# Kernel tuning notes

Measured on AMD Instinct MI355X. Metric: run time of the kernel, lower is better.

## Reference

```python
import jax, jax.numpy as jnp
import numpy as np

B, T, C = 2, 2048, 1024
H = 16
HD = C // H  # 64


def setup_inputs() -> dict:
    key = jax.random.key(0)
    ks = jax.random.split(key, 6)
    s_in = 1.0 / np.sqrt(C)
    s_pr = 1.0 / np.sqrt(H * HD)
    x = jax.random.normal(ks[0], (B, T, C), dtype=jnp.float32)
    Wq = jax.random.uniform(ks[1], (H, C, HD), jnp.float32, -s_in, s_in)
    Wk = jax.random.uniform(ks[2], (H, C, HD), jnp.float32, -s_in, s_in)
    Wv = jax.random.uniform(ks[3], (H, C, HD), jnp.float32, -s_in, s_in)
    Wp = jax.random.uniform(ks[4], (H * HD, C), jnp.float32, -s_pr, s_pr)
    bp = jax.random.uniform(ks[5], (C,), jnp.float32, -s_pr, s_pr)
    return {"x": x, "Wq": Wq, "Wk": Wk, "Wv": Wv, "Wp": Wp, "bp": bp}


def reference(x, Wq, Wk, Wv, Wp, bp):
    # per-head projections: [B,T,C] x [H,C,D] -> [B,H,T,D]
    q = jnp.einsum('btc,hcd->bhtd', x, Wq)
    k = jnp.einsum('btc,hcd->bhtd', x, Wk)
    v = jnp.einsum('btc,hcd->bhtd', x, Wv)
    scale = HD ** (-0.5)
    scores = jnp.einsum('bhtd,bhsd->bhts', q, k) * scale  # [B,H,T,T]
    causal = jnp.tril(jnp.ones((T, T), dtype=bool))
    scores = jnp.where(causal, scores, -jnp.inf)
    w = jax.nn.softmax(scores, axis=-1)
    out = jnp.einsum('bhts,bhsd->bhtd', w, v)  # [B,H,T,D]
    # concat heads: [B,T,H*D] (head order matches torch.cat over heads)
    out = jnp.transpose(out, (0, 2, 1, 3)).reshape(B, T, H * HD)
    return out @ Wp + bp
```

## Files before the change

### kernel.cpp

```cpp
#include <hip/hip_runtime.h>
#include <hip/hip_bf16.h>

#define B_NUM 2
#define T_SEQ 2048
#define C_DIM 1024
#define H_NUM 16
#define HD    64
#define M_TOT 4096
#define BH_N  32

typedef __attribute__((ext_vector_type(8))) short short8;
typedef __attribute__((ext_vector_type(4))) float floatx4;

__device__ __forceinline__ short f2bf(float f) {
    unsigned u = __float_as_uint(f);
    u += 0x7FFFu + ((u >> 16) & 1u);
    return (short)(u >> 16);
}

__device__ __forceinline__ unsigned pk2bf(float a, float b) {
    float2 f2; f2.x = a; f2.y = b;
    __hip_bfloat162 h = __float22bfloat162_rn(f2);
    unsigned u; __builtin_memcpy(&u, &h, 4); return u;
}

__device__ __forceinline__ void gld16(const short* g, short* l) {
    __builtin_amdgcn_global_load_lds(
        (const __attribute__((address_space(1))) void*)g,
        (__attribute__((address_space(3))) void*)l, 16, 0, 0);
}

__global__ __launch_bounds__(256) void prep_k(
    const float* __restrict__ x, const float* __restrict__ Wq,
    const float* __restrict__ Wk, const float* __restrict__ Wv,
    const float* __restrict__ Wp,
    short* __restrict__ xb, short* __restrict__ wt, short* __restrict__ wpt) {
    const int bid = blockIdx.x;
    const int tid = threadIdx.x;
    if (bid < 2048) {
        int idx = (bid * 256 + tid) * 8;
        float4 a = *(const float4*)(x + idx);
        float4 b = *(const float4*)(x + idx + 4);
        short8 o;
        o[0] = f2bf(a.x); o[1] = f2bf(a.y); o[2] = f2bf(a.z); o[3] = f2bf(a.w);
        o[4] = f2bf(b.x); o[5] = f2bf(b.y); o[6] = f2bf(b.z); o[7] = f2bf(b.w);
        *(short8*)(xb + idx) = o;
        return;
    }
    const int b2 = bid - 2048;
    const int ct = b2 & 15, y = b2 >> 4;
    __shared__ float shf[4096];

    const float* src;
    size_t src_stride;
    int src_col0;
    short* dst;
    int dst_col0;
    if (y < 48) {
        const int which = y >> 4, h = y & 15;
        src = ((which == 0) ? Wq : (which == 1) ? Wk : Wv)
              + (size_t)h * C_DIM * HD + (size_t)(ct * 64) * HD;
        src_stride = HD;  src_col0 = 0;
        dst = wt + (size_t)((which * 16 + h) * 64) * C_DIM;
        dst_col0 = ct * 64;
    } else {
        const int nt = y - 48;
        src = Wp + (size_t)(ct * 64) * C_DIM;
        src_stride = C_DIM;  src_col0 = nt * 64;
        dst = wpt + (size_t)(nt * 64) * C_DIM;
        dst_col0 = ct * 64;
    }
    #pragma unroll
    for (int p = 0; p < 4; ++p) {
        int idx = tid + 256 * p;
        int c = idx >> 4, d4 = idx & 15;
        float4 v = *(const float4*)(src + (size_t)c * src_stride + src_col0 + d4 * 4);
        shf[(d4 * 4 + 0) * 64 + (c ^ (d4 * 4 + 0))] = v.x;
        shf[(d4 * 4 + 1) * 64 + (c ^ (d4 * 4 + 1))] = v.y;
        shf[(d4 * 4 + 2) * 64 + (c ^ (d4 * 4 + 2))] = v.z;
        shf[(d4 * 4 + 3) * 64 + (c ^ (d4 * 4 + 3))] = v.w;
    }
    __syncthreads();
    #pragma unroll
    for (int p = 0; p < 2; ++p) {
        int idx = tid + 256 * p;
        int d = idx >> 3, cc = idx & 7;
        const float* row = shf + d * 64;
        uint4 u;
        u.x = pk2bf(row[(cc * 8 + 0) ^ d], row[(cc * 8 + 1) ^ d]);
        u.y = pk2bf(row[(cc * 8 + 2) ^ d], row[(cc * 8 + 3) ^ d]);
        u.z = pk2bf(row[(cc * 8 + 4) ^ d], row[(cc * 8 + 5) ^ d]);
        u.w = pk2bf(row[(cc * 8 + 6) ^ d], row[(cc * 8 + 7) ^ d]);
        *(uint4*)(dst + (size_t)d * C_DIM + dst_col0 + cc * 8) = u;
    }
}

__global__ __launch_bounds__(512, 2) void qkv_k(
    const short* __restrict__ xb, const short* __restrict__ wt,
    short* __restrict__ qb, short* __restrict__ kb, short* __restrict__ vtb) {
    const int swz = (blockIdx.x & 7) * 24 + (blockIdx.x >> 3);
    const int mt = swz / 12, ntg = swz % 12;
    const int m0 = mt * 256, n0 = ntg * 256;
    const int which = n0 >> 10;
    const float sc = (which == 0) ? 0.125f * 1.4426950408889634f : 1.0f;

    __shared__ short smem[32768];
    short* As = smem;
    short* Bs = smem + 16384;

    const int tid = threadIdx.x;
    const int lane = tid & 63, w = tid >> 6;
    const int wm = w & 1, wn = w >> 1;
    const int hi = lane >> 4, llo = lane & 15;
    const int lrow = lane >> 3;
    const int lswz = ((lane & 7) ^ (lrow & 7)) * 8;
    const int fc0 = (hi ^ (llo & 7)) * 8;
    const int fc1 = ((hi + 4) ^ (llo & 7)) * 8;

    floatx4 acc[8][4];
    #pragma unroll
    for (int i = 0; i < 8; ++i)
        #pragma unroll
        for (int j = 0; j < 4; ++j)
            #pragma unroll
            for (int r = 0; r < 4; ++r) acc[i][j][r] = 0.0f;

    const size_t a_base = (size_t)(m0 + w * 32 + lrow) * C_DIM + lswz;
    const size_t b_base = (size_t)(n0 + w * 32 + lrow) * C_DIM + lswz;

    for (int kt = 0; kt < C_DIM / 64; ++kt) {
        const int c0 = kt * 64;
        __syncthreads();
        #pragma unroll
        for (int p = 0; p < 4; ++p) {
            gld16(xb + a_base + (size_t)p * 8 * C_DIM + c0, &As[(w * 32 + p * 8) * 64]);
            gld16(wt + b_base + (size_t)p * 8 * C_DIM + c0, &Bs[(w * 32 + p * 8) * 64]);
        }
        __syncthreads();

        short8 bf[4][2];
        #pragma unroll
        for (int ni = 0; ni < 4; ++ni) {
            const int row = wn * 64 + ni * 16 + llo;
            bf[ni][0] = *(const short8*)(&Bs[row * 64 + fc0]);
            bf[ni][1] = *(const short8*)(&Bs[row * 64 + fc1]);
        }
        #pragma unroll
        for (int mi = 0; mi < 8; ++mi) {
            const int row = wm * 128 + mi * 16 + llo;
            short8 a0 = *(const short8*)(&As[row * 64 + fc0]);
            short8 a1 = *(const short8*)(&As[row * 64 + fc1]);
            #pragma unroll
            for (int ni = 0; ni < 4; ++ni) {
                acc[mi][ni] = __builtin_amdgcn_mfma_f32_16x16x32_bf16(a0, bf[ni][0], acc[mi][ni], 0, 0, 0);
                acc[mi][ni] = __builtin_amdgcn_mfma_f32_16x16x32_bf16(a1, bf[ni][1], acc[mi][ni], 0, 0, 0);
            }
        }
    }

    const int bb = m0 >> 11;
    if (which < 2) {
        short (*R)[76] = (short(*)[76])smem;
        short* outp = (which == 0) ? qb : kb;
        #pragma unroll
        for (int c = 0; c < 4; ++c) {
            __syncthreads();
            if (wn == c) {
                #pragma unroll
                for (int mi = 0; mi < 8; ++mi)
                    #pragma unroll
                    for (int ni = 0; ni < 4; ++ni)
                        #pragma unroll
                        for (int r = 0; r < 4; ++r)
                            R[wm * 128 + mi * 16 + hi * 4 + r][ni * 16 + llo] =
                                f2bf(acc[mi][ni][r] * sc);
            }
            __syncthreads();
            const int h = ((n0 + c * 64) >> 6) & 15;
            #pragma unroll
            for (int p = 0; p < 4; ++p) {
                int idx = tid + 512 * p;
                int r = idx >> 3, cc = idx & 7;
                short8 vv = *(const short8*)(&R[r][cc * 8]);
                int t = (m0 + r) & 2047;
                *(short8*)(outp + ((size_t)(bb * H_NUM + h) * T_SEQ + t) * HD + cc * 8) = vv;
            }
        }
    } else {
        short (*R2)[268] = (short(*)[268])smem;
        #pragma unroll
        for (int c = 0; c < 4; ++c) {
            __syncthreads();
            if (wn == c) {
                #pragma unroll
                for (int mi = 0; mi < 8; ++mi)
                    #pragma unroll
                    for (int ni = 0; ni < 4; ++ni)
                        #pragma unroll
                        for (int r = 0; r < 4; ++r)
                            R2[ni * 16 + llo][wm * 128 + mi * 16 + hi * 4 + r] =
                                f2bf(acc[mi][ni][r]);
            }
            __syncthreads();
            const int h = ((n0 + c * 64) >> 6) & 15;
            #pragma unroll
            for (int p = 0; p < 4; ++p) {
                int idx = tid + 512 * p;
                int d = idx >> 5, cc = idx & 31;
                short8 vv = *(const short8*)(&R2[d][cc * 8]);
                *(short8*)(vtb + ((size_t)((bb * H_NUM + h) * HD + d)) * T_SEQ
                           + (m0 & 2047) + cc * 8) = vv;
            }
        }
    }
}

__global__ __launch_bounds__(512) void attn_k(
    const short* __restrict__ qb, const short* __restrict__ kb,
    const short* __restrict__ vtb, short* __restrict__ attb) {
    const int bh = blockIdx.x;
    const int y = blockIdx.y;
    const int qt = (y < 8) ? (15 - y) : (y - 8);
    const int b = bh >> 4, h = bh & 15;
    const short* K  = kb  + (size_t)bh * T_SEQ * HD;
    const short* Vt = vtb + (size_t)bh * HD * T_SEQ;

    __shared__ short Ks[2][4096];
    __shared__ short Vs[2][4096];
    __shared__ short Ps[128][76];

    const int tid = threadIdx.x;
    const int lane = tid & 63, w = tid >> 6;
    const int hi = lane >> 4, llo = lane & 15;
    const int lrow = lane >> 3;
    const int lswz = ((lane & 7) ^ (lrow & 7)) * 8;
    const int fc0 = (hi ^ (llo & 7)) * 8;
    const int fc1 = ((hi + 4) ^ (llo & 7)) * 8;
    const int kmax = 2 * qt + 1;

    short8 qf[2];
    const int qcol0 = qt * 128 + w * 16;
    #pragma unroll
    for (int kh = 0; kh < 2; ++kh)
        qf[kh] = *(const short8*)(qb +
            ((size_t)bh * T_SEQ + qcol0 + llo) * HD + kh * 32 + hi * 8);

    short8 av4;
    #pragma unroll
    for (int j = 0; j < 8; ++j) av4[j] = (llo == 0) ? (short)0x3F80 : (short)0;

    gld16(K + (size_t)(w * 8 + lrow) * HD + lswz, &Ks[0][(w * 8) * 64]);
    gld16(Vt + (size_t)(w * 8 + lrow) * T_SEQ + lswz, &Vs[0][(w * 8) * 64]);

    floatx4 Oa[5];
    #pragma unroll
    for (int n = 0; n < 5; ++n)
        #pragma unroll
        for (int r = 0; r < 4; ++r) Oa[n][r] = 0.0f;

    for (int kt = 0; kt <= kmax; ++kt) {
        __syncthreads();
        const int buf = kt & 1;

        if (kt + 1 <= kmax) {
            const int s0 = (kt + 1) * 64;
            const int nb = buf ^ 1;
            gld16(K + ((size_t)s0 + w * 8 + lrow) * HD + lswz, &Ks[nb][(w * 8) * 64]);
            gld16(Vt + (size_t)(w * 8 + lrow) * T_SEQ + s0 + lswz, &Vs[nb][(w * 8) * 64]);
        }

        short8 ak[4][2];
        #pragma unroll
        for (int nt = 0; nt < 4; ++nt) {
            const int row = nt * 16 + llo;
            ak[nt][0] = *(const short8*)(&Ks[buf][row * 64 + fc0]);
            ak[nt][1] = *(const short8*)(&Ks[buf][row * 64 + fc1]);
        }
        floatx4 sf[4];
        #pragma unroll
        for (int nt = 0; nt < 4; ++nt)
            #pragma unroll
            for (int r = 0; r < 4; ++r) sf[nt][r] = 0.0f;
        __builtin_amdgcn_s_setprio(1);
        #pragma unroll
        for (int nt = 0; nt < 4; ++nt)
            #pragma unroll
            for (int kh = 0; kh < 2; ++kh)
                sf[nt] = __builtin_amdgcn_mfma_f32_16x16x32_bf16(
                    ak[nt][kh], qf[kh], sf[nt], 0, 0, 0);
        __builtin_amdgcn_s_setprio(0);

        const int sbase = kt * 64;
        if (sbase + 63 > qcol0) {
            const int qlane = qcol0 + llo;
            #pragma unroll
            for (int nt = 0; nt < 4; ++nt)
                #pragma unroll
                for (int r = 0; r < 4; ++r)
                    if (sbase + nt * 16 + hi * 4 + r > qlane) sf[nt][r] = -3.0e38f;
        }

        #pragma unroll
        for (int nt = 0; nt < 4; ++nt) {
            float p0 = __builtin_amdgcn_exp2f(sf[nt][0]);
            float p1 = __builtin_amdgcn_exp2f(sf[nt][1]);
            float p2 = __builtin_amdgcn_exp2f(sf[nt][2]);
            float p3 = __builtin_amdgcn_exp2f(sf[nt][3]);
            uint2 u; u.x = pk2bf(p0, p1); u.y = pk2bf(p2, p3);
            *(uint2*)(&Ps[w * 16 + llo][nt * 16 + hi * 4]) = u;
        }

        short8 av[5][2];
        #pragma unroll
        for (int nt2 = 0; nt2 < 4; ++nt2) {
            const int row = nt2 * 16 + llo;
            av[nt2][0] = *(const short8*)(&Vs[buf][row * 64 + fc0]);
            av[nt2][1] = *(const short8*)(&Vs[buf][row * 64 + fc1]);
        }
        av[4][0] = av4;
        av[4][1] = av4;
        short8 bpf[2];
        #pragma unroll
        for (int kh = 0; kh < 2; ++kh)
            bpf[kh] = *(const short8*)(&Ps[w * 16 + llo][kh * 32 + hi * 8]);
        __builtin_amdgcn_s_setprio(1);
        #pragma unroll
        for (int nt2 = 0; nt2 < 5; ++nt2)
            #pragma unroll
            for (int kh = 0; kh < 2; ++kh)
                Oa[nt2] = __builtin_amdgcn_mfma_f32_16x16x32_bf16(
                    av[nt2][kh], bpf[kh], Oa[nt2], 0, 0, 0);
        __builtin_amdgcn_s_setprio(0);
    }

    {
        float lb = __shfl(Oa[4][0], llo);
        float inv = 1.0f / lb;
        #pragma unroll
        for (int nt2 = 0; nt2 < 4; ++nt2) {
            uint2 u;
            u.x = pk2bf(Oa[nt2][0] * inv, Oa[nt2][1] * inv);
            u.y = pk2bf(Oa[nt2][2] * inv, Oa[nt2][3] * inv);
            *(uint2*)(&Ps[w * 16 + llo][nt2 * 16 + hi * 4]) = u;
        }
    }
    __syncthreads();
    #pragma unroll
    for (int p = 0; p < 2; ++p) {
        int idx = tid + 512 * p;
        int r = idx >> 3, cc = idx & 7;
        short8 vv = *(const short8*)(&Ps[r][cc * 8]);
        *(short8*)(attb + ((size_t)(b * T_SEQ + qt * 128 + r)) * C_DIM + h * HD + cc * 8) = vv;
    }
}

__global__ __launch_bounds__(256) void proj_k(
    const short* __restrict__ attb, const short* __restrict__ wpt,
    const float* __restrict__ bp, float* __restrict__ out) {
    const int mt = blockIdx.x, ntg = blockIdx.y;
    const int m0 = mt * 128, n0 = ntg * 128;

    __shared__ short smem[16384];
    short* As = smem;
    short* Bs = smem + 8192;

    const int tid = threadIdx.x;
    const int lane = tid & 63, w = tid >> 6;
    const int wm = w & 1, wn = w >> 1;
    const int hi = lane >> 4, llo = lane & 15;
    const int lrow = lane >> 3;
    const int lswz = ((lane & 7) ^ (lrow & 7)) * 8;
    const int fc0 = (hi ^ (llo & 7)) * 8;
    const int fc1 = ((hi + 4) ^ (llo & 7)) * 8;

    floatx4 acc[4][4];
    #pragma unroll
    for (int i = 0; i < 4; ++i)
        #pragma unroll
        for (int j = 0; j < 4; ++j)
            #pragma unroll
            for (int r = 0; r < 4; ++r) acc[i][j][r] = 0.0f;

    const size_t a_base = (size_t)(m0 + w * 32 + lrow) * C_DIM + lswz;
    const size_t b_base = (size_t)(n0 + w * 32 + lrow) * C_DIM + lswz;

    for (int kt = 0; kt < C_DIM / 64; ++kt) {
        const int c0 = kt * 64;
        __syncthreads();
        #pragma unroll
        for (int p = 0; p < 4; ++p) {
            gld16(attb + a_base + (size_t)p * 8 * C_DIM + c0, &As[(w * 32 + p * 8) * 64]);
            gld16(wpt  + b_base + (size_t)p * 8 * C_DIM + c0, &Bs[(w * 32 + p * 8) * 64]);
        }
        __syncthreads();

        short8 af[4][2];
        #pragma unroll
        for (int mi = 0; mi < 4; ++mi) {
            const int row = wm * 64 + mi * 16 + llo;
            af[mi][0] = *(const short8*)(&As[row * 64 + fc0]);
            af[mi][1] = *(const short8*)(&As[row * 64 + fc1]);
        }
        #pragma unroll
        for (int ni = 0; ni < 4; ++ni) {
            const int row = wn * 64 + ni * 16 + llo;
            short8 b0 = *(const short8*)(&Bs[row * 64 + fc0]);
            short8 b1 = *(const short8*)(&Bs[row * 64 + fc1]);
            #pragma unroll
            for (int mi = 0; mi < 4; ++mi) {
                acc[mi][ni] = __builtin_amdgcn_mfma_f32_16x16x32_bf16(af[mi][0], b0, acc[mi][ni], 0, 0, 0);
                acc[mi][ni] = __builtin_amdgcn_mfma_f32_16x16x32_bf16(af[mi][1], b1, acc[mi][ni], 0, 0, 0);
            }
        }
    }

    #pragma unroll
    for (int ni = 0; ni < 4; ++ni) {
        const int n = n0 + wn * 64 + ni * 16 + llo;
        const float bias = bp[n];
        #pragma unroll
        for (int mi = 0; mi < 4; ++mi)
            #pragma unroll
            for (int r = 0; r < 4; ++r) {
                int m = m0 + wm * 64 + mi * 16 + hi * 4 + r;
                out[(size_t)m * C_DIM + n] = acc[mi][ni][r] + bias;
            }
    }
}

extern "C" void kernel_launch(void* const* d_in, const int* in_sizes, int n_in,
                              void* d_out, int out_size, void* d_ws, size_t ws_size,
                              hipStream_t stream) {
    const float* x  = (const float*)d_in[0];
    const float* Wq = (const float*)d_in[1];
    const float* Wk = (const float*)d_in[2];
    const float* Wv = (const float*)d_in[3];
    const float* Wp = (const float*)d_in[4];
    const float* bp = (const float*)d_in[5];
    float* out = (float*)d_out;

    short* xb   = (short*)d_ws;
    short* wt   = xb  + (size_t)M_TOT * C_DIM;
    short* wpt  = wt  + (size_t)3 * H_NUM * HD * C_DIM;
    short* qb   = wpt + (size_t)C_DIM * C_DIM;
    short* kb   = qb  + (size_t)M_TOT * C_DIM;
    short* vtb  = kb  + (size_t)M_TOT * C_DIM;
    short* attb = vtb + (size_t)M_TOT * C_DIM;

    prep_k<<<dim3(3072), 256, 0, stream>>>(x, Wq, Wk, Wv, Wp, xb, wt, wpt);
    qkv_k <<<dim3(192), 512, 0, stream>>>(xb, wt, qb, kb, vtb);
    attn_k<<<dim3(BH_N, T_SEQ / 128), 512, 0, stream>>>(qb, kb, vtb, attb);
    proj_k<<<dim3(M_TOT / 128, C_DIM / 128), 256, 0, stream>>>(attb, wpt, bp, out);
}
```

Before: 189.2 us.

## Double-buffer LDS in QKV and projection GEMMs, retile QKV to 256 blocks

Both GEMM kernels now use two shared-memory buffers and prefetch the next K-tile while MFMAs run on the current one, which removes one barrier per iteration and overlaps global loads with compute. The QKV GEMM also switches its N tile from 256 to 192 columns, so the grid grows from 192 to 256 blocks and better fills the CUs. Its epilogue now handles tiles that can straddle head and Q/K/V boundaries, choosing per 64-column chunk. QKV uses 112KB of dynamic LDS at one block per CU, which lowers occupancy.

```diff
diff --git a/kernel.cpp b/kernel.cpp
--- a/kernel.cpp
+++ b/kernel.cpp
@@ -95,18 +95,14 @@
     }
 }
 
-__global__ __launch_bounds__(512, 2) void qkv_k(
+__global__ __launch_bounds__(512, 1) void qkv_k(
     const short* __restrict__ xb, const short* __restrict__ wt,
     short* __restrict__ qb, short* __restrict__ kb, short* __restrict__ vtb) {
-    const int swz = (blockIdx.x & 7) * 24 + (blockIdx.x >> 3);
-    const int mt = swz / 12, ntg = swz % 12;
-    const int m0 = mt * 256, n0 = ntg * 256;
-    const int which = n0 >> 10;
-    const float sc = (which == 0) ? 0.125f * 1.4426950408889634f : 1.0f;
-
-    __shared__ short smem[32768];
-    short* As = smem;
-    short* Bs = smem + 16384;
+    extern __shared__ short smem[];
+
+    const int swz = (blockIdx.x & 7) * 32 + (blockIdx.x >> 3);
+    const int mt = swz >> 4, ntg = swz & 15;
+    const int m0 = mt * 256, n0 = ntg * 192;
 
     const int tid = threadIdx.x;
     const int lane = tid & 63, w = tid >> 6;
@@ -117,31 +113,43 @@
     const int fc0 = (hi ^ (llo & 7)) * 8;
     const int fc1 = ((hi + 4) ^ (llo & 7)) * 8;
 
-    floatx4 acc[8][4];
+    floatx4 acc[8][3];
     #pragma unroll
     for (int i = 0; i < 8; ++i)
         #pragma unroll
-        for (int j = 0; j < 4; ++j)
+        for (int j = 0; j < 3; ++j)
             #pragma unroll
             for (int r = 0; r < 4; ++r) acc[i][j][r] = 0.0f;
 
     const size_t a_base = (size_t)(m0 + w * 32 + lrow) * C_DIM + lswz;
-    const size_t b_base = (size_t)(n0 + w * 32 + lrow) * C_DIM + lswz;
-
-    for (int kt = 0; kt < C_DIM / 64; ++kt) {
+    const size_t b_base = (size_t)(n0 + w * 24 + lrow) * C_DIM + lswz;
+
+    auto STAGE = [&](int bsel, int kt) {
         const int c0 = kt * 64;
-        __syncthreads();
-        #pragma unroll
-        for (int p = 0; p < 4; ++p) {
-            gld16(xb + a_base + (size_t)p * 8 * C_DIM + c0, &As[(w * 32 + p * 8) * 64]);
-            gld16(wt + b_base + (size_t)p * 8 * C_DIM + c0, &Bs[(w * 32 + p * 8) * 64]);
-        }
-        __syncthreads();
-
-        short8 bf[4][2];
-        #pragma unroll
-        for (int ni = 0; ni < 4; ++ni) {
-            const int row = wn * 64 + ni * 16 + llo;
+        short* Ad = smem + bsel * 16384;
+        short* Bd = smem + 32768 + bsel * 12288;
+        #pragma unroll
+        for (int p = 0; p < 4; ++p)
+            gld16(xb + a_base + (size_t)p * 8 * C_DIM + c0, &Ad[(w * 32 + p * 8) * 64]);
+        #pragma unroll
+        for (int p = 0; p < 3; ++p)
+            gld16(wt + b_base + (size_t)p * 8 * C_DIM + c0, &Bd[(w * 24 + p * 8) * 64]);
+    };
+
+    STAGE(0, 0);
+    __syncthreads();
+
+    for (int kt = 0; kt < 16; ++kt) {
+        const int cur = kt & 1;
+        if (kt < 15) STAGE(cur ^ 1, kt + 1);
+
+        const short* As = smem + cur * 16384;
+        const short* Bs = smem + 32768 + cur * 12288;
+
+        short8 bf[3][2];
+        #pragma unroll
+        for (int ni = 0; ni < 3; ++ni) {
+            const int row = wn * 48 + ni * 16 + llo;
             bf[ni][0] = *(const short8*)(&Bs[row * 64 + fc0]);
             bf[ni][1] = *(const short8*)(&Bs[row * 64 + fc1]);
         }
@@ -151,58 +159,36 @@
             short8 a0 = *(const short8*)(&As[row * 64 + fc0]);
             short8 a1 = *(const short8*)(&As[row * 64 + fc1]);
             #pragma unroll
-            for (int ni = 0; ni < 4; ++ni) {
+            for (int ni = 0; ni < 3; ++ni) {
                 acc[mi][ni] = __builtin_amdgcn_mfma_f32_16x16x32_bf16(a0, bf[ni][0], acc[mi][ni], 0, 0, 0);
                 acc[mi][ni] = __builtin_amdgcn_mfma_f32_16x16x32_bf16(a1, bf[ni][1], acc[mi][ni], 0, 0, 0);
             }
         }
+        __syncthreads();
     }
 
     const int bb = m0 >> 11;
-    if (which < 2) {
-        short (*R)[76] = (short(*)[76])smem;
-        short* outp = (which == 0) ? qb : kb;
-        #pragma unroll
-        for (int c = 0; c < 4; ++c) {
-            __syncthreads();
-            if (wn == c) {
-                #pragma unroll
-                for (int mi = 0; mi < 8; ++mi)
+    #pragma unroll
+    for (int c = 0; c < 3; ++c) {
+        const int nch = n0 + c * 64;
+        const int which = nch >> 10;
+        const int h = (nch >> 6) & 15;
+        __syncthreads();
+        if (which == 2) {
+            short (*R2)[268] = (short(*)[268])smem;
+            #pragma unroll
+            for (int ni = 0; ni < 3; ++ni) {
+                const int gcol = wn * 48 + ni * 16;
+                if ((gcol >> 6) == c) {
                     #pragma unroll
-                    for (int ni = 0; ni < 4; ++ni)
+                    for (int mi = 0; mi < 8; ++mi)
                         #pragma unroll
                         for (int r = 0; r < 4; ++r)
-                            R[wm * 128 + mi * 16 + hi * 4 + r][ni * 16 + llo] =
-                                f2bf(acc[mi][ni][r] * sc);
+                            R2[(gcol & 63) + llo][wm * 128 + mi * 16 + hi * 4 + r] =
+                                f2bf(acc[mi][ni][r]);
+                }
             }
             __syncthreads();
-            const int h = ((n0 + c * 64) >> 6) & 15;
-            #pragma unroll
-            for (int p = 0; p < 4; ++p) {
-                int idx = tid + 512 * p;
-                int r = idx >> 3, cc = idx & 7;
-                short8 vv = *(const short8*)(&R[r][cc * 8]);
-                int t = (m0 + r) & 2047;
-                *(short8*)(outp + ((size_t)(bb * H_NUM + h) * T_SEQ + t) * HD + cc * 8) = vv;
-            }
-        }
-    } else {
-        short (*R2)[268] = (short(*)[268])smem;
-        #pragma unroll
-        for (int c = 0; c < 4; ++c) {
-            __syncthreads();
-            if (wn == c) {
-                #pragma unroll
-                for (int mi = 0; mi < 8; ++mi)
-                    #pragma unroll
-                    for (int ni = 0; ni < 4; ++ni)
-                        #pragma unroll
-                        for (int r = 0; r < 4; ++r)
-                            R2[ni * 16 + llo][wm * 128 + mi * 16 + hi * 4 + r] =
-                                f2bf(acc[mi][ni][r]);
-            }
-            __syncthreads();
-            const int h = ((n0 + c * 64) >> 6) & 15;
             #pragma unroll
             for (int p = 0; p < 4; ++p) {
                 int idx = tid + 512 * p;
@@ -210,6 +196,31 @@
                 short8 vv = *(const short8*)(&R2[d][cc * 8]);
                 *(short8*)(vtb + ((size_t)((bb * H_NUM + h) * HD + d)) * T_SEQ
                            + (m0 & 2047) + cc * 8) = vv;
+            }
+        } else {
+            short (*R)[76] = (short(*)[76])smem;
+            const float scl = (which == 0) ? 0.125f * 1.4426950408889634f : 1.0f;
+            short* outp = (which == 0) ? qb : kb;
+            #pragma unroll
+            for (int ni = 0; ni < 3; ++ni) {
+                const int gcol = wn * 48 + ni * 16;
+                if ((gcol >> 6) == c) {
+                    #pragma unroll
+                    for (int mi = 0; mi < 8; ++mi)
+                        #pragma unroll
+                        for (int r = 0; r < 4; ++r)
+                            R[wm * 128 + mi * 16 + hi * 4 + r][(gcol & 63) + llo] =
+                                f2bf(acc[mi][ni][r] * scl);
+                }
+            }
+            __syncthreads();
+            #pragma unroll
+            for (int p = 0; p < 4; ++p) {
+                int idx = tid + 512 * p;
+                int rr = idx >> 3, cc = idx & 7;
+                short8 vv = *(const short8*)(&R[rr][cc * 8]);
+                int t = (m0 + rr) & 2047;
+                *(short8*)(outp + ((size_t)(bb * H_NUM + h) * T_SEQ + t) * HD + cc * 8) = vv;
             }
         }
     }
@@ -360,9 +371,7 @@
     const int mt = blockIdx.x, ntg = blockIdx.y;
     const int m0 = mt * 128, n0 = ntg * 128;
 
-    __shared__ short smem[16384];
-    short* As = smem;
-    short* Bs = smem + 8192;
+    __shared__ short smem[32768];
 
     const int tid = threadIdx.x;
     const int lane = tid & 63, w = tid >> 6;
@@ -384,15 +393,26 @@
     const size_t a_base = (size_t)(m0 + w * 32 + lrow) * C_DIM + lswz;
     const size_t b_base = (size_t)(n0 + w * 32 + lrow) * C_DIM + lswz;
 
-    for (int kt = 0; kt < C_DIM / 64; ++kt) {
+    auto STAGE = [&](int bsel, int kt) {
         const int c0 = kt * 64;
-        __syncthreads();
+        short* Ad = smem + bsel * 8192;
+        short* Bd = smem + 16384 + bsel * 8192;
         #pragma unroll
         for (int p = 0; p < 4; ++p) {
-            gld16(attb + a_base + (size_t)p * 8 * C_DIM + c0, &As[(w * 32 + p * 8) * 64]);
-            gld16(wpt  + b_base + (size_t)p * 8 * C_DIM + c0, &Bs[(w * 32 + p * 8) * 64]);
-        }
-        __syncthreads();
+            gld16(attb + a_base + (size_t)p * 8 * C_DIM + c0, &Ad[(w * 32 + p * 8) * 64]);
+            gld16(wpt  + b_base + (size_t)p * 8 * C_DIM + c0, &Bd[(w * 32 + p * 8) * 64]);
+        }
+    };
+
+    STAGE(0, 0);
+    __syncthreads();
+
+    for (int kt = 0; kt < 16; ++kt) {
+        const int cur = kt & 1;
+        if (kt < 15) STAGE(cur ^ 1, kt + 1);
+
+        const short* As = smem + cur * 8192;
+        const short* Bs = smem + 16384 + cur * 8192;
 
         short8 af[4][2];
         #pragma unroll
@@ -412,6 +432,7 @@
                 acc[mi][ni] = __builtin_amdgcn_mfma_f32_16x16x32_bf16(af[mi][1], b1, acc[mi][ni], 0, 0, 0);
             }
         }
+        __syncthreads();
     }
 
     #pragma unroll
@@ -447,8 +468,16 @@
     short* vtb  = kb  + (size_t)M_TOT * C_DIM;
     short* attb = vtb + (size_t)M_TOT * C_DIM;
 
+    static bool attr_done = false;
+    if (!attr_done) {
+        (void)hipFuncSetAttribute((const void*)qkv_k,
+                                  hipFuncAttributeMaxDynamicSharedMemorySize,
+                                  114688);
+        attr_done = true;
+    }
+
     prep_k<<<dim3(3072), 256, 0, stream>>>(x, Wq, Wk, Wv, Wp, xb, wt, wpt);
-    qkv_k <<<dim3(192), 512, 0, stream>>>(xb, wt, qb, kb, vtb);
+    qkv_k <<<dim3(256), 512, 114688, stream>>>(xb, wt, qb, kb, vtb);
     attn_k<<<dim3(BH_N, T_SEQ / 128), 512, 0, stream>>>(qb, kb, vtb, attb);
     proj_k<<<dim3(M_TOT / 128, C_DIM / 128), 256, 0, stream>>>(attb, wpt, bp, out);
 }
```

Measured after the change: 167.7 us. 1.13x faster.
